# Kernel tuning notes

Measured on AMD Instinct MI355X. Metric: run time of the kernel, lower is better.

## Reference

```python
import jax, jax.numpy as jnp
import numpy as np

B, S, K, D = 2048, 32, 1024, 64
DECAY = 0.9
LOG_2PI = float(np.log(2.0 * np.pi))


def _gmm_log_probs(slots, mu, log_sigma):
    """log N(slots | mu_k, sigma_k) summed over feature dim -> [B, S, K].

    Expanded quadratic form avoids materializing the [B,S,K,D] broadcast:
    -0.5 * sum_d (x-mu)^2/var - sum_d log sigma - 0.5*D*log(2*pi)
    """
    inv_var = jnp.exp(-2.0 * log_sigma)                      # [K, D]
    x2 = jnp.einsum('bsd,kd->bsk', slots * slots, inv_var)    # sum x^2/var
    xm = jnp.einsum('bsd,kd->bsk', slots, mu * inv_var)       # sum x*mu/var
    m2 = jnp.sum(mu * mu * inv_var, axis=-1)                  # [K]
    const = jnp.sum(log_sigma, axis=-1) + 0.5 * D * LOG_2PI   # [K]
    return -0.5 * (x2 - 2.0 * xm + m2) - const


def setup_inputs() -> dict:
    key = jax.random.key(0)
    k0, k1, k2, k3 = jax.random.split(key, 4)
    return {
        'slots': jax.random.normal(k0, (B, S, D), dtype=jnp.float32),
        'mu': jax.random.normal(k1, (K, D), dtype=jnp.float32),
        'log_sigma': jax.random.normal(k2, (K, D), dtype=jnp.float32),
        'log_prior': jnp.zeros((K,), dtype=jnp.float32),
        'z': jax.random.normal(k3, (B, S, D), dtype=jnp.float32),
    }


def reference(slots, mu, log_sigma, log_prior, z):
    sigma = jnp.exp(log_sigma)                                # [K, D]
    log_probs = _gmm_log_probs(slots, mu, log_sigma)          # [B, S, K]
    responsibilities = jax.nn.softmax(log_probs, axis=-1)     # [B, S, K]
    # argmax of responsibilities == argmax of log_probs (softmax is monotone)
    assignments = jnp.argmax(log_probs, axis=-1)              # [B, S] int
    new_slots = mu[assignments] + sigma[assignments] * z      # [B, S, D]
    log_likelihood = jnp.take_along_axis(
        log_probs, assignments[..., None], axis=-1)[..., 0]   # [B, S]
    # EMA prior update (non-trainable buffer in the original module)
    new_log_prior = (DECAY * jax.nn.softmax(log_prior)
                     + (1.0 - DECAY) * jax.nn.softmax(
                         jnp.sum(responsibilities, axis=(0, 1))))
    return new_slots, log_likelihood, new_log_prior
```

## Files before the change

kernel.cpp:

```cpp
#include <hip/hip_runtime.h>
#include <math.h>

#define KK 1024
#define DD 64
#define BS 65536
#define TM 64
#define NBLK (BS/TM)
#define NTHR 512
#define LN_2PI 1.8378770664093453f
#define DECAY 0.9f
#define APAD 136

typedef _Float16 f16x8 __attribute__((ext_vector_type(8)));
typedef float f32x4 __attribute__((ext_vector_type(4)));

#define BH_OFF   0
#define BL_OFF   65536
#define C_OFF    131072
#define SIG_OFF  (C_OFF + KK)
#define RESP_OFF (SIG_OFF + KK*DD)

__global__ __launch_bounds__(64) void prep_kernel(
    const float* __restrict__ mu, const float* __restrict__ log_sigma,
    float* __restrict__ ws) {
  int k = blockIdx.x;
  int d = threadIdx.x;
  float ls = log_sigma[k*DD + d];
  float m  = mu[k*DD + d];
  float iv = expf(-2.0f*ls);
  _Float16* Bh = (_Float16*)(ws + BH_OFF);
  _Float16* Bl = (_Float16*)(ws + BL_OFF);
  {
    float w0 = -0.5f*iv;
    _Float16 h = (_Float16)w0;
    int dd = d;
    Bh[((size_t)(dd >> 3)*KK + k)*8 + (dd & 7)] = h;
    Bl[((size_t)(dd >> 3)*KK + k)*8 + (dd & 7)] = (_Float16)(w0 - (float)h);
  }
  {
    float w1 = m*iv;
    _Float16 h = (_Float16)w1;
    int dd = 64 + d;
    Bh[((size_t)(dd >> 3)*KK + k)*8 + (dd & 7)] = h;
    Bl[((size_t)(dd >> 3)*KK + k)*8 + (dd & 7)] = (_Float16)(w1 - (float)h);
  }
  ws[SIG_OFF + k*DD + d] = expf(ls);
  float t1 = m*m*iv;
  float t2 = ls;
  #pragma unroll
  for (int off = 32; off; off >>= 1) {
    t1 += __shfl_xor(t1, off);
    t2 += __shfl_xor(t2, off);
  }
  if (d == 0) ws[C_OFF + k] = -0.5f*t1 - t2 - 32.0f*LN_2PI;
}

__global__ __launch_bounds__(512, 2) void main_kernel(
    const float* __restrict__ slots, const float* __restrict__ mu,
    const float* __restrict__ z, const float* __restrict__ ws,
    float* __restrict__ out_slots, float* __restrict__ out_ll,
    float* __restrict__ resp_g) {
  __shared__ _Float16 Ah[TM][APAD];
  __shared__ _Float16 Al[TM][APAD];
  __shared__ float mxl[TM][8];
  __shared__ int   ail[TM][8];
  __shared__ float sml[TM][8];
  __shared__ float gm_l[TM];
  __shared__ float inv_l[TM];
  __shared__ int   am_l[TM];
  __shared__ float resl[KK];

  const int t    = threadIdx.x;
  const int lane = t & 63;
  const int w    = t >> 6;
  const int lg   = lane >> 4;
  const int lc   = lane & 15;
  const int R0   = blockIdx.x * TM;

  {
    int row = t >> 3;
    int dp  = (t & 7) * 8;
    float4 v0 = *(const float4*)(slots + (size_t)(R0 + row)*DD + dp);
    float4 v1 = *(const float4*)(slots + (size_t)(R0 + row)*DD + dp + 4);
    float f[8] = {v0.x, v0.y, v0.z, v0.w, v1.x, v1.y, v1.z, v1.w};
    f16x8 sqh, sql, sh, sl;
    #pragma unroll
    for (int j = 0; j < 8; ++j) {
      float sq = f[j]*f[j];
      _Float16 h1 = (_Float16)sq;
      sqh[j] = h1; sql[j] = (_Float16)(sq - (float)h1);
      _Float16 h2 = (_Float16)f[j];
      sh[j] = h2;  sl[j]  = (_Float16)(f[j] - (float)h2);
    }
    *(f16x8*)&Ah[row][dp]      = sqh;
    *(f16x8*)&Al[row][dp]      = sql;
    *(f16x8*)&Ah[row][64 + dp] = sh;
    *(f16x8*)&Al[row][64 + dp] = sl;
  }
  __syncthreads();

  const f16x8* BH = (const f16x8*)(ws + BH_OFF);
  const f16x8* BL = (const f16x8*)(ws + BL_OFF);
  const float* Cc = ws + C_OFF;
  const int colbase = (w << 7) + lc;

  f32x4 acc[4][8];
  #pragma unroll
  for (int ct = 0; ct < 8; ++ct) {
    float c = Cc[colbase + ct*16];
    #pragma unroll
    for (int rg = 0; rg < 4; ++rg) acc[rg][ct] = (f32x4){c, c, c, c};
  }

  #pragma unroll
  for (int s = 0; s < 4; ++s) {
    const int kb = s*32 + lg*8;
    f16x8 ah[4], al[4];
    #pragma unroll
    for (int rg = 0; rg < 4; ++rg) {
      ah[rg] = *(const f16x8*)&Ah[rg*16 + lc][kb];
      al[rg] = *(const f16x8*)&Al[rg*16 + lc][kb];
    }
    const int kblk = s*4 + lg;
    #pragma unroll
    for (int ct = 0; ct < 8; ++ct) {
      int col = (w << 7) + ct*16 + lc;
      f16x8 bh = BH[(size_t)kblk*KK + col];
      f16x8 bl = BL[(size_t)kblk*KK + col];
      #pragma unroll
      for (int rg = 0; rg < 4; ++rg) {
        acc[rg][ct] = __builtin_amdgcn_mfma_f32_16x16x32_f16(ah[rg], bh, acc[rg][ct], 0, 0, 0);
        acc[rg][ct] = __builtin_amdgcn_mfma_f32_16x16x32_f16(ah[rg], bl, acc[rg][ct], 0, 0, 0);
        acc[rg][ct] = __builtin_amdgcn_mfma_f32_16x16x32_f16(al[rg], bh, acc[rg][ct], 0, 0, 0);
      }
    }
  }

  #pragma unroll
  for (int rg = 0; rg < 4; ++rg) {
    #pragma unroll
    for (int q = 0; q < 4; ++q) {
      float m = acc[rg][0][q];
      int  mi = colbase;
      #pragma unroll
      for (int ct = 1; ct < 8; ++ct) {
        if (acc[rg][ct][q] > m) { m = acc[rg][ct][q]; mi = colbase + ct*16; }
      }
      #pragma unroll
      for (int off = 1; off < 16; off <<= 1) {
        float om = __shfl_xor(m, off);
        int   oi = __shfl_xor(mi, off);
        if (om > m || (om == m && oi < mi)) { m = om; mi = oi; }
      }
      if (lc == 0) {
        int row = rg*16 + lg*4 + q;
        mxl[row][w] = m; ail[row][w] = mi;
      }
    }
  }
  __syncthreads();

  if (t < TM) {
    float m = mxl[t][0]; int mi = ail[t][0];
    #pragma unroll
    for (int g = 1; g < 8; ++g) {
      float om = mxl[t][g]; int oi = ail[t][g];
      if (om > m || (om == m && oi < mi)) { m = om; mi = oi; }
    }
    gm_l[t] = m; am_l[t] = mi;
    out_ll[R0 + t] = m;
  }
  __syncthreads();

  float gmv[4][4];
  #pragma unroll
  for (int rg = 0; rg < 4; ++rg)
    #pragma unroll
    for (int q = 0; q < 4; ++q) gmv[rg][q] = gm_l[rg*16 + lg*4 + q];

  #pragma unroll
  for (int rg = 0; rg < 4; ++rg) {
    #pragma unroll
    for (int q = 0; q < 4; ++q) {
      float sacc = 0.0f;
      #pragma unroll
      for (int ct = 0; ct < 8; ++ct) {
        float e = __expf(acc[rg][ct][q] - gmv[rg][q]);
        acc[rg][ct][q] = e;
        sacc += e;
      }
      #pragma unroll
      for (int off = 1; off < 16; off <<= 1) sacc += __shfl_xor(sacc, off);
      if (lc == 0) sml[rg*16 + lg*4 + q][w] = sacc;
    }
  }
  __syncthreads();
  if (t < TM) {
    float s = 0.0f;
    #pragma unroll
    for (int g = 0; g < 8; ++g) s += sml[t][g];
    inv_l[t] = 1.0f / s;
  }
  __syncthreads();

  {
    float invv[4][4];
    #pragma unroll
    for (int rg = 0; rg < 4; ++rg)
      #pragma unroll
      for (int q = 0; q < 4; ++q) invv[rg][q] = inv_l[rg*16 + lg*4 + q];
    float rc[8];
    #pragma unroll
    for (int ct = 0; ct < 8; ++ct) {
      float s = 0.0f;
      #pragma unroll
      for (int rg = 0; rg < 4; ++rg)
        #pragma unroll
        for (int q = 0; q < 4; ++q) s += acc[rg][ct][q] * invv[rg][q];
      rc[ct] = s;
    }
    #pragma unroll
    for (int ct = 0; ct < 8; ++ct) {
      rc[ct] += __shfl_xor(rc[ct], 16);
      rc[ct] += __shfl_xor(rc[ct], 32);
    }
    if (lane < 16) {
      #pragma unroll
      for (int ct = 0; ct < 8; ++ct) resl[(w << 7) + ct*16 + lane] = rc[ct];
    }
  }
  __syncthreads();
  for (int c = t; c < KK; c += NTHR) atomicAdd(resp_g + c, resl[c]);

  {
    int row = t >> 3;
    int dp  = (t & 7) * 8;
    int a = am_l[row];
    #pragma unroll
    for (int h = 0; h < 2; ++h) {
      int d0 = dp + h*4;
      float4 zv = *(const float4*)(z  + (size_t)(R0 + row)*DD + d0);
      float4 mv = *(const float4*)(mu + (size_t)a*DD + d0);
      float4 sg = *(const float4*)(ws + SIG_OFF + (size_t)a*DD + d0);
      float4 o;
      o.x = fmaf(sg.x, zv.x, mv.x);
      o.y = fmaf(sg.y, zv.y, mv.y);
      o.z = fmaf(sg.z, zv.z, mv.z);
      o.w = fmaf(sg.w, zv.w, mv.w);
      *(float4*)(out_slots + (size_t)(R0 + row)*DD + d0) = o;
    }
  }
}

__device__ __forceinline__ float block_max_1024(float v, float* red) {
  #pragma unroll
  for (int off = 32; off; off >>= 1) v = fmaxf(v, __shfl_xor(v, off));
  int wave = threadIdx.x >> 6, lane = threadIdx.x & 63;
  if (lane == 0) red[wave] = v;
  __syncthreads();
  float m = red[0];
  #pragma unroll
  for (int w = 1; w < 16; ++w) m = fmaxf(m, red[w]);
  __syncthreads();
  return m;
}

__device__ __forceinline__ float block_sum_1024(float v, float* red) {
  #pragma unroll
  for (int off = 32; off; off >>= 1) v += __shfl_xor(v, off);
  int wave = threadIdx.x >> 6, lane = threadIdx.x & 63;
  if (lane == 0) red[wave] = v;
  __syncthreads();
  float s = 0.0f;
  #pragma unroll
  for (int w = 0; w < 16; ++w) s += red[w];
  __syncthreads();
  return s;
}

__global__ __launch_bounds__(1024) void finalize_kernel(
    const float* __restrict__ log_prior, const float* __restrict__ resp_g,
    float* __restrict__ out_prior) {
  __shared__ float red[16];
  int t = threadIdx.x;
  float lp = log_prior[t];
  float rs = resp_g[t];

  float m1 = block_max_1024(lp, red);
  float e1 = __expf(lp - m1);
  float s1 = block_sum_1024(e1, red);

  float m2 = block_max_1024(rs, red);
  float e2 = __expf(rs - m2);
  float s2 = block_sum_1024(e2, red);

  out_prior[t] = DECAY * (e1 / s1) + (1.0f - DECAY) * (e2 / s2);
}

extern "C" void kernel_launch(void* const* d_in, const int* in_sizes, int n_in,
                              void* d_out, int out_size, void* d_ws, size_t ws_size,
                              hipStream_t stream) {
  const float* slots     = (const float*)d_in[0];
  const float* mu        = (const float*)d_in[1];
  const float* log_sigma = (const float*)d_in[2];
  const float* log_prior = (const float*)d_in[3];
  const float* z         = (const float*)d_in[4];

  float* out       = (float*)d_out;
  float* out_slots = out;
  float* out_ll    = out + (size_t)BS*DD;
  float* out_prior = out + (size_t)BS*DD + BS;
  float* ws        = (float*)d_ws;

  hipMemsetAsync(ws + RESP_OFF, 0, KK*sizeof(float), stream);
  prep_kernel<<<KK, 64, 0, stream>>>(mu, log_sigma, ws);
  main_kernel<<<NBLK, NTHR, 0, stream>>>(slots, mu, z, ws, out_slots, out_ll,
                                         ws + RESP_OFF);
  finalize_kernel<<<1, 1024, 0, stream>>>(log_prior, ws + RESP_OFF, out_prior);
}
```

Measured before the change: 115.9 us.

## Switch GMM scoring to 32x32x16 MFMA with B-fragment prefetch and direct atomics

Replaces the 16x16x32 MFMA tiling with 32x32x16 MFMA tiles (2 row groups × 4 column tiles per wave), so each B fragment loaded from global memory is reused across more rows. The next k-step's B fragments are prefetched into registers while the current MFMAs run. The shared-memory column-sum staging buffer and its barrier are removed in favor of per-lane atomicAdd. The z/mu/sigma gather loads for the output are issued earlier to overlap with the softmax reductions. The cost is higher register pressure from the prefetch buffers and early loads, plus longer 32-lane shuffle reductions.

New measurement: 164.6 us. 1.42x slower.

```diff
diff --git a/kernel.cpp b/kernel.cpp
--- a/kernel.cpp
+++ b/kernel.cpp
@@ -12,7 +12,7 @@
 #define APAD 136
 
 typedef _Float16 f16x8 __attribute__((ext_vector_type(8)));
-typedef float f32x4 __attribute__((ext_vector_type(4)));
+typedef float f32x16 __attribute__((ext_vector_type(16)));
 
 #define BH_OFF   0
 #define BL_OFF   65536
@@ -32,17 +32,16 @@
   _Float16* Bl = (_Float16*)(ws + BL_OFF);
   {
     float w0 = -0.5f*iv;
-    _Float16 h = (_Float16)w0;
-    int dd = d;
-    Bh[((size_t)(dd >> 3)*KK + k)*8 + (dd & 7)] = h;
-    Bl[((size_t)(dd >> 3)*KK + k)*8 + (dd & 7)] = (_Float16)(w0 - (float)h);
+    _Float16 hh = (_Float16)w0;
+    Bh[((size_t)(d >> 3)*KK + k)*8 + (d & 7)] = hh;
+    Bl[((size_t)(d >> 3)*KK + k)*8 + (d & 7)] = (_Float16)(w0 - (float)hh);
   }
   {
     float w1 = m*iv;
-    _Float16 h = (_Float16)w1;
+    _Float16 hh = (_Float16)w1;
     int dd = 64 + d;
-    Bh[((size_t)(dd >> 3)*KK + k)*8 + (dd & 7)] = h;
-    Bl[((size_t)(dd >> 3)*KK + k)*8 + (dd & 7)] = (_Float16)(w1 - (float)h);
+    Bh[((size_t)(dd >> 3)*KK + k)*8 + (dd & 7)] = hh;
+    Bl[((size_t)(dd >> 3)*KK + k)*8 + (dd & 7)] = (_Float16)(w1 - (float)hh);
   }
   ws[SIG_OFF + k*DD + d] = expf(ls);
   float t1 = m*m*iv;
@@ -68,13 +67,12 @@
   __shared__ float gm_l[TM];
   __shared__ float inv_l[TM];
   __shared__ int   am_l[TM];
-  __shared__ float resl[KK];
 
   const int t    = threadIdx.x;
   const int lane = t & 63;
   const int w    = t >> 6;
-  const int lg   = lane >> 4;
-  const int lc   = lane & 15;
+  const int h    = lane >> 5;
+  const int lc   = lane & 31;
   const int R0   = blockIdx.x * TM;
 
   {
@@ -101,59 +99,73 @@
 
   const f16x8* BH = (const f16x8*)(ws + BH_OFF);
   const f16x8* BL = (const f16x8*)(ws + BL_OFF);
-  const float* Cc = ws + C_OFF;
-  const int colbase = (w << 7) + lc;
-
-  f32x4 acc[4][8];
-  #pragma unroll
-  for (int ct = 0; ct < 8; ++ct) {
-    float c = Cc[colbase + ct*16];
-    #pragma unroll
-    for (int rg = 0; rg < 4; ++rg) acc[rg][ct] = (f32x4){c, c, c, c};
-  }
-
-  #pragma unroll
-  for (int s = 0; s < 4; ++s) {
-    const int kb = s*32 + lg*8;
-    f16x8 ah[4], al[4];
-    #pragma unroll
-    for (int rg = 0; rg < 4; ++rg) {
-      ah[rg] = *(const f16x8*)&Ah[rg*16 + lc][kb];
-      al[rg] = *(const f16x8*)&Al[rg*16 + lc][kb];
-    }
-    const int kblk = s*4 + lg;
-    #pragma unroll
-    for (int ct = 0; ct < 8; ++ct) {
-      int col = (w << 7) + ct*16 + lc;
-      f16x8 bh = BH[(size_t)kblk*KK + col];
-      f16x8 bl = BL[(size_t)kblk*KK + col];
-      #pragma unroll
-      for (int rg = 0; rg < 4; ++rg) {
-        acc[rg][ct] = __builtin_amdgcn_mfma_f32_16x16x32_f16(ah[rg], bh, acc[rg][ct], 0, 0, 0);
-        acc[rg][ct] = __builtin_amdgcn_mfma_f32_16x16x32_f16(ah[rg], bl, acc[rg][ct], 0, 0, 0);
-        acc[rg][ct] = __builtin_amdgcn_mfma_f32_16x16x32_f16(al[rg], bh, acc[rg][ct], 0, 0, 0);
-      }
-    }
-  }
-
-  #pragma unroll
-  for (int rg = 0; rg < 4; ++rg) {
-    #pragma unroll
-    for (int q = 0; q < 4; ++q) {
+  const int col0 = (w << 7) + lc;
+  const f16x8* pH = BH + (size_t)h*KK + col0;
+  const f16x8* pL = BL + (size_t)h*KK + col0;
+
+  f32x16 acc[2][4];
+  {
+    const float* Cc = ws + C_OFF;
+    #pragma unroll
+    for (int ct = 0; ct < 4; ++ct) {
+      float cv = Cc[col0 + ct*32];
+      f32x16 ini;
+      #pragma unroll
+      for (int j = 0; j < 16; ++j) ini[j] = cv;
+      acc[0][ct] = ini; acc[1][ct] = ini;
+    }
+  }
+
+  f16x8 bh[4], bl[4];
+  #pragma unroll
+  for (int ct = 0; ct < 4; ++ct) { bh[ct] = pH[ct*32]; bl[ct] = pL[ct*32]; }
+
+  #pragma unroll
+  for (int s = 0; s < 8; ++s) {
+    f16x8 ah0 = *(const f16x8*)&Ah[lc     ][s*16 + h*8];
+    f16x8 al0 = *(const f16x8*)&Al[lc     ][s*16 + h*8];
+    f16x8 ah1 = *(const f16x8*)&Ah[32 + lc][s*16 + h*8];
+    f16x8 al1 = *(const f16x8*)&Al[32 + lc][s*16 + h*8];
+    f16x8 nh[4], nl[4];
+    if (s < 7) {
+      #pragma unroll
+      for (int ct = 0; ct < 4; ++ct) {
+        nh[ct] = pH[(s+1)*2*KK + ct*32];
+        nl[ct] = pL[(s+1)*2*KK + ct*32];
+      }
+    }
+    #pragma unroll
+    for (int ct = 0; ct < 4; ++ct) {
+      acc[0][ct] = __builtin_amdgcn_mfma_f32_32x32x16_f16(ah0, bh[ct], acc[0][ct], 0, 0, 0);
+      acc[1][ct] = __builtin_amdgcn_mfma_f32_32x32x16_f16(ah1, bh[ct], acc[1][ct], 0, 0, 0);
+      acc[0][ct] = __builtin_amdgcn_mfma_f32_32x32x16_f16(ah0, bl[ct], acc[0][ct], 0, 0, 0);
+      acc[1][ct] = __builtin_amdgcn_mfma_f32_32x32x16_f16(ah1, bl[ct], acc[1][ct], 0, 0, 0);
+      acc[0][ct] = __builtin_amdgcn_mfma_f32_32x32x16_f16(al0, bh[ct], acc[0][ct], 0, 0, 0);
+      acc[1][ct] = __builtin_amdgcn_mfma_f32_32x32x16_f16(al1, bh[ct], acc[1][ct], 0, 0, 0);
+    }
+    if (s < 7) {
+      #pragma unroll
+      for (int ct = 0; ct < 4; ++ct) { bh[ct] = nh[ct]; bl[ct] = nl[ct]; }
+    }
+  }
+
+  #pragma unroll
+  for (int rg = 0; rg < 2; ++rg) {
+    #pragma unroll
+    for (int q = 0; q < 16; ++q) {
       float m = acc[rg][0][q];
-      int  mi = colbase;
-      #pragma unroll
-      for (int ct = 1; ct < 8; ++ct) {
-        if (acc[rg][ct][q] > m) { m = acc[rg][ct][q]; mi = colbase + ct*16; }
-      }
-      #pragma unroll
-      for (int off = 1; off < 16; off <<= 1) {
+      int  mi = col0;
+      #pragma unroll
+      for (int ct = 1; ct < 4; ++ct)
+        if (acc[rg][ct][q] > m) { m = acc[rg][ct][q]; mi = col0 + ct*32; }
+      #pragma unroll
+      for (int off = 1; off < 32; off <<= 1) {
         float om = __shfl_xor(m, off);
         int   oi = __shfl_xor(mi, off);
         if (om > m || (om == m && oi < mi)) { m = om; mi = oi; }
       }
       if (lc == 0) {
-        int row = rg*16 + lg*4 + q;
+        int row = rg*32 + (q&3) + 8*(q>>2) + 4*h;
         mxl[row][w] = m; ail[row][w] = mi;
       }
     }
@@ -172,83 +184,71 @@
   }
   __syncthreads();
 
-  float gmv[4][4];
-  #pragma unroll
-  for (int rg = 0; rg < 4; ++rg)
-    #pragma unroll
-    for (int q = 0; q < 4; ++q) gmv[rg][q] = gm_l[rg*16 + lg*4 + q];
-
-  #pragma unroll
-  for (int rg = 0; rg < 4; ++rg) {
-    #pragma unroll
-    for (int q = 0; q < 4; ++q) {
+  const int frow = t >> 3;
+  const int fdp  = (t & 7) * 8;
+  const int fa   = am_l[frow];
+  const float* zr = z  + (size_t)(R0 + frow)*DD + fdp;
+  const float* mr = mu + (size_t)fa*DD + fdp;
+  const float* sr = ws + SIG_OFF + (size_t)fa*DD + fdp;
+  float4 fz0 = *(const float4*)zr,     fz1 = *(const float4*)(zr + 4);
+  float4 fm0 = *(const float4*)mr,     fm1 = *(const float4*)(mr + 4);
+  float4 fs0 = *(const float4*)sr,     fs1 = *(const float4*)(sr + 4);
+
+  #pragma unroll
+  for (int rg = 0; rg < 2; ++rg) {
+    #pragma unroll
+    for (int q = 0; q < 16; ++q) {
+      int row = rg*32 + (q&3) + 8*(q>>2) + 4*h;
+      float gm = gm_l[row];
       float sacc = 0.0f;
       #pragma unroll
-      for (int ct = 0; ct < 8; ++ct) {
-        float e = __expf(acc[rg][ct][q] - gmv[rg][q]);
+      for (int ct = 0; ct < 4; ++ct) {
+        float e = __expf(acc[rg][ct][q] - gm);
         acc[rg][ct][q] = e;
         sacc += e;
       }
       #pragma unroll
-      for (int off = 1; off < 16; off <<= 1) sacc += __shfl_xor(sacc, off);
-      if (lc == 0) sml[rg*16 + lg*4 + q][w] = sacc;
+      for (int off = 1; off < 32; off <<= 1) sacc += __shfl_xor(sacc, off);
+      if (lc == 0) sml[row][w] = sacc;
     }
   }
   __syncthreads();
   if (t < TM) {
-    float s = 0.0f;
-    #pragma unroll
-    for (int g = 0; g < 8; ++g) s += sml[t][g];
-    inv_l[t] = 1.0f / s;
-  }
-  __syncthreads();
-
-  {
-    float invv[4][4];
-    #pragma unroll
-    for (int rg = 0; rg < 4; ++rg)
-      #pragma unroll
-      for (int q = 0; q < 4; ++q) invv[rg][q] = inv_l[rg*16 + lg*4 + q];
-    float rc[8];
-    #pragma unroll
-    for (int ct = 0; ct < 8; ++ct) {
-      float s = 0.0f;
-      #pragma unroll
-      for (int rg = 0; rg < 4; ++rg)
+    float ssum = 0.0f;
+    #pragma unroll
+    for (int g = 0; g < 8; ++g) ssum += sml[t][g];
+    inv_l[t] = 1.0f / ssum;
+  }
+  __syncthreads();
+
+  {
+    float rc[4] = {0.0f, 0.0f, 0.0f, 0.0f};
+    #pragma unroll
+    for (int rg = 0; rg < 2; ++rg) {
+      #pragma unroll
+      for (int q = 0; q < 16; ++q) {
+        int row = rg*32 + (q&3) + 8*(q>>2) + 4*h;
+        float inv = inv_l[row];
         #pragma unroll
-        for (int q = 0; q < 4; ++q) s += acc[rg][ct][q] * invv[rg][q];
-      rc[ct] = s;
-    }
-    #pragma unroll
-    for (int ct = 0; ct < 8; ++ct) {
-      rc[ct] += __shfl_xor(rc[ct], 16);
-      rc[ct] += __shfl_xor(rc[ct], 32);
-    }
-    if (lane < 16) {
-      #pragma unroll
-      for (int ct = 0; ct < 8; ++ct) resl[(w << 7) + ct*16 + lane] = rc[ct];
-    }
-  }
-  __syncthreads();
-  for (int c = t; c < KK; c += NTHR) atomicAdd(resp_g + c, resl[c]);
-
-  {
-    int row = t >> 3;
-    int dp  = (t & 7) * 8;
-    int a = am_l[row];
-    #pragma unroll
-    for (int h = 0; h < 2; ++h) {
-      int d0 = dp + h*4;
-      float4 zv = *(const float4*)(z  + (size_t)(R0 + row)*DD + d0);
-      float4 mv = *(const float4*)(mu + (size_t)a*DD + d0);
-      float4 sg = *(const float4*)(ws + SIG_OFF + (size_t)a*DD + d0);
-      float4 o;
-      o.x = fmaf(sg.x, zv.x, mv.x);
-      o.y = fmaf(sg.y, zv.y, mv.y);
-      o.z = fmaf(sg.z, zv.z, mv.z);
-      o.w = fmaf(sg.w, zv.w, mv.w);
-      *(float4*)(out_slots + (size_t)(R0 + row)*DD + d0) = o;
-    }
+        for (int ct = 0; ct < 4; ++ct) rc[ct] += acc[rg][ct][q] * inv;
+      }
+    }
+    #pragma unroll
+    for (int ct = 0; ct < 4; ++ct) rc[ct] += __shfl_xor(rc[ct], 32);
+    if (lane < 32) {
+      #pragma unroll
+      for (int ct = 0; ct < 4; ++ct) atomicAdd(resp_g + col0 + ct*32, rc[ct]);
+    }
+  }
+
+  {
+    float4 o0, o1;
+    o0.x = fmaf(fs0.x, fz0.x, fm0.x); o0.y = fmaf(fs0.y, fz0.y, fm0.y);
+    o0.z = fmaf(fs0.z, fz0.z, fm0.z); o0.w = fmaf(fs0.w, fz0.w, fm0.w);
+    o1.x = fmaf(fs1.x, fz1.x, fm1.x); o1.y = fmaf(fs1.y, fz1.y, fm1.y);
+    o1.z = fmaf(fs1.z, fz1.z, fm1.z); o1.w = fmaf(fs1.w, fz1.w, fm1.w);
+    *(float4*)(out_slots + (size_t)(R0 + frow)*DD + fdp)     = o0;
+    *(float4*)(out_slots + (size_t)(R0 + frow)*DD + fdp + 4) = o1;
   }
 }
 
```
